# Optimization experiments

Hardware: AMD Instinct MI355X
Metric: run time of the kernel (lower is better)

The kernel has to match this reference:

```python
import jax, jax.numpy as jnp
import numpy as np

B, D, K = 8, 128, 7          # batch, num objects, per-object feature
Q = 256                      # question embedding size
G0, G1 = 511, 512            # g-layer sizes
F1, F2, OUT = 512, 1024, 16  # f-layer sizes


def setup_inputs() -> dict:
    key = jax.random.key(0)
    ks = jax.random.split(key, 14)
    def lin(kw, kb, fan_in, fan_out):
        lim = 1.0 / np.sqrt(fan_in)
        w = jax.random.uniform(kw, (fan_in, fan_out), jnp.float32, -lim, lim)
        b = jax.random.uniform(kb, (fan_out,), jnp.float32, -lim, lim)
        return w, b
    x = jax.random.normal(ks[0], (B, D, K), jnp.float32)
    qst = jax.random.normal(ks[1], (B, Q), jnp.float32)
    g0_w, g0_b = lin(ks[2], ks[3], 2 * K, G0)
    g1_w, g1_b = lin(ks[4], ks[5], G0 + Q, G1)
    f1_w, f1_b = lin(ks[6], ks[7], G1, F1)
    f2_w, f2_b = lin(ks[8], ks[9], F1, F2)
    f3_w, f3_b = lin(ks[10], ks[11], F2, OUT)
    return {"x": x, "qst": qst,
            "g0_w": g0_w, "g0_b": g0_b, "g1_w": g1_w, "g1_b": g1_b,
            "f1_w": f1_w, "f1_b": f1_b, "f2_w": f2_w, "f2_b": f2_b,
            "f3_w": f3_w, "f3_b": f3_b}


def reference(x, qst, g0_w, g0_b, g1_w, g1_b, f1_w, f1_b, f2_w, f2_b, f3_w, f3_b):
    b, d, k = x.shape
    # all-pairs: torch x_i[b,a,c,:]=x[b,c,:], x_j[b,a,c,:]=x[b,a,:]
    x_i = jnp.broadcast_to(x[:, None, :, :], (b, d, d, k))
    x_j = jnp.broadcast_to(x[:, :, None, :], (b, d, d, k))
    pairs = jnp.concatenate([x_i, x_j], axis=-1)            # (b,d,d,2k)
    h = jax.nn.relu(pairs @ g0_w + g0_b)                    # (b,d,d,G0)
    q = jnp.broadcast_to(qst[:, None, None, :], (b, d, d, qst.shape[-1]))
    h = jnp.concatenate([h, q], axis=-1)                    # (b,d,d,G0+Q)
    h = jax.nn.relu(h @ g1_w + g1_b)                        # (b,d,d,G1)
    x_g = h.sum(axis=(1, 2))                                # sum over d^2 pairs -> (b,G1)
    f = jax.nn.relu(x_g @ f1_w + f1_b)
    f = jax.nn.relu(f @ f2_w + f2_b)                        # dropout = identity (eval)
    logits = f @ f3_w + f3_b
    return jax.nn.log_softmax(logits, axis=1)
```

## Files before the change

### kernel.cpp

```cpp
#include <hip/hip_runtime.h>
#include <hip/hip_bf16.h>

#define B_  8
#define D_  128
#define K_  7
#define Q_  256
#define G0_ 511
#define G0P 512
#define G1_ 512
#define F1_ 512
#define F2_ 1024
#define OUT_ 16

typedef __bf16 bf16x8 __attribute__((ext_vector_type(8)));
typedef float  f32x4  __attribute__((ext_vector_type(4)));

#define GL2LDS(g, l) __builtin_amdgcn_global_load_lds(                        \
    (const __attribute__((address_space(1))) void*)(g),                       \
    (__attribute__((address_space(3))) void*)(l), 16, 0, 0)

__global__ void k_prep(const float* __restrict__ x, const float* __restrict__ g0w,
                       const float* __restrict__ g0b, const float* __restrict__ qst,
                       const float* __restrict__ g1w, const float* __restrict__ g1b,
                       const float* __restrict__ f1w, const float* __restrict__ f2w,
                       const float* __restrict__ f3w,
                       float* __restrict__ u, float* __restrict__ v,
                       __bf16* __restrict__ w1t, float* __restrict__ qterm,
                       float* __restrict__ xg, float* __restrict__ f1t,
                       float* __restrict__ f2t, float* __restrict__ f3t) {
    const int blk = blockIdx.x;
    const int t   = threadIdx.x;
    if (blk < 1024) {
        __shared__ float xs[8];
        if (t < K_) xs[t] = x[blk * K_ + t];
        __syncthreads();
        #pragma unroll
        for (int h = 0; h < 2; ++h) {
            const int g = t + h * 256;
            float su = 0.f, sv = 0.f;
            if (g < G0_) {
                #pragma unroll
                for (int k = 0; k < K_; ++k) {
                    su += xs[k] * g0w[k * G0_ + g];
                    sv += xs[k] * g0w[(K_ + k) * G0_ + g];
                }
                su += g0b[g];
            }
            u[blk * G0P + g] = (g < G0_) ? su : 0.f;
            v[blk * G0P + g] = (g < G0_) ? sv : 0.f;
        }
    } else if (blk < 1280) {
        __shared__ __bf16 tile[32][33];
        const int bb = blk - 1024;
        const int bx = bb & 15, by = bb >> 4;
        const int r = t >> 5, c = t & 31;
        #pragma unroll
        for (int i = 0; i < 4; ++i) {
            const int k = by * 32 + r + i * 8;
            const int n = bx * 32 + c;
            tile[r + i * 8][c] = (__bf16)((k < G0_) ? g1w[k * G1_ + n] : 0.f);
        }
        __syncthreads();
        #pragma unroll
        for (int i = 0; i < 4; ++i) {
            const int n = bx * 32 + r + i * 8;
            const int cc = (c >> 3) & 3, j = c & 7;
            const int slot = cc ^ ((n >> 1) & 3);
            w1t[by * 16384 + n * 32 + slot * 8 + j] = tile[c][r + i * 8];
        }
    } else if (blk < 1312) {
        __shared__ float qs[256];
        __shared__ float red[2][128];
        const int qb = blk - 1280;
        const int b = qb >> 2, nb = (qb & 3) << 7;
        qs[t] = qst[b * Q_ + t];
        __syncthreads();
        const int n = nb + (t & 127);
        const int qh = (t >> 7) * 128;
        float s = 0.f;
        #pragma unroll 8
        for (int q = 0; q < 128; ++q)
            s += qs[qh + q] * g1w[(G0_ + qh + q) * G1_ + n];
        red[t >> 7][t & 127] = s;
        __syncthreads();
        if (t < 128)
            qterm[b * G1_ + nb + t] = red[0][t] + red[1][t] + g1b[nb + t];
    } else if (blk < 1320) {
        const int b = blk - 1312;
        xg[b * G1_ + t] = 0.f;
        xg[b * G1_ + 256 + t] = 0.f;
    } else if (blk < 1576) {
        __shared__ float tile[32][33];
        const int j = blk - 1320;
        const int bo = j & 15, bk = j >> 4;
        const int r = t >> 5, c = t & 31;
        #pragma unroll
        for (int i = 0; i < 4; ++i)
            tile[r + i * 8][c] = f1w[(bk * 32 + r + i * 8) * F1_ + bo * 32 + c];
        __syncthreads();
        #pragma unroll
        for (int i = 0; i < 4; ++i)
            f1t[(bo * 32 + r + i * 8) * G1_ + bk * 32 + c] = tile[c][r + i * 8];
    } else if (blk < 2088) {
        __shared__ float tile[32][33];
        const int j = blk - 1576;
        const int bo = j & 31, bk = j >> 5;
        const int r = t >> 5, c = t & 31;
        #pragma unroll
        for (int i = 0; i < 4; ++i)
            tile[r + i * 8][c] = f2w[(bk * 32 + r + i * 8) * F2_ + bo * 32 + c];
        __syncthreads();
        #pragma unroll
        for (int i = 0; i < 4; ++i)
            f2t[(bo * 32 + r + i * 8) * F1_ + bk * 32 + c] = tile[c][r + i * 8];
    } else {
        const int k = (blk - 2088) * 256 + t;
        float4 r0 = *(const float4*)(f3w + k * OUT_);
        float4 r1 = *(const float4*)(f3w + k * OUT_ + 4);
        float4 r2 = *(const float4*)(f3w + k * OUT_ + 8);
        float4 r3 = *(const float4*)(f3w + k * OUT_ + 12);
        const float rr[16] = {r0.x,r0.y,r0.z,r0.w, r1.x,r1.y,r1.z,r1.w,
                              r2.x,r2.y,r2.z,r2.w, r3.x,r3.y,r3.z,r3.w};
        #pragma unroll
        for (int o = 0; o < 16; ++o) f3t[o * F2_ + k] = rr[o];
    }
}

__global__ __launch_bounds__(256, 2)
void k_pair(const float* __restrict__ u, const float* __restrict__ v,
            const __bf16* __restrict__ w1t, const float* __restrict__ qterm,
            float* __restrict__ xg) {
    __shared__ float  v_a[512];
    __shared__ __bf16 At[2][4096];
    __shared__ __bf16 Bt[3][8192];
    __shared__ float  ebuf[4][128];

    const int bid  = blockIdx.x;
    const int b    = bid >> 8;
    const int a    = (bid >> 1) & 127;
    const int nbase = (bid & 1) << 8;
    const int tid  = threadIdx.x;
    const int wave = tid >> 6, lane = tid & 63;
    const int quad = lane >> 4, l15 = lane & 15;
    const int nloc = (wave >> 1) * 128;
    const int mtg  = (wave & 1) * 4;
    const int swz  = (l15 >> 1) & 3;

    const int iw0 = wave * 4;
    const __bf16* gsrc = w1t + (size_t)(nbase + iw0 * 16 + (lane >> 2)) * 32
                             + (lane & 3) * 8;

    const int sm = tid >> 1;
    const int sk = (tid & 1) << 4;
    const float* urow = u + (b * D_ + sm) * G0P + sk;
    const int woff = (sm >> 4) * 512 + (sk >> 3) * 128 + (sm & 15) * 8;

    f32x4 acc[4][8];
    #pragma unroll
    for (int mt = 0; mt < 4; ++mt)
        #pragma unroll
        for (int nt = 0; nt < 8; ++nt)
            acc[mt][nt] = (f32x4){0.f, 0.f, 0.f, 0.f};

    float4 u0, u1, u2, u3;
    auto load_u = [&](int kq) {
        const float* p = urow + kq * 32;
        u0 = *(const float4*)p;       u1 = *(const float4*)(p + 4);
        u2 = *(const float4*)(p + 8); u3 = *(const float4*)(p + 12);
    };
    auto stage_B = [&](int buf, int kq) {
        const __bf16* g = gsrc + kq * 16384;
        __bf16* l = &Bt[buf][iw0 * 512];
        #pragma unroll
        for (int j = 0; j < 4; ++j)
            GL2LDS(g + j * 512, l + j * 512);
    };
    auto write_A = [&](int buf, int kq) {
        const float* vp = v_a + kq * 32 + sk;
        const float4 v0 = *(const float4*)vp,       v1 = *(const float4*)(vp + 4);
        const float4 v2 = *(const float4*)(vp + 8), v3 = *(const float4*)(vp + 12);
        bf16x8 h0, h1;
        h0[0] = (__bf16)fmaxf(u0.x + v0.x, 0.f);
        h0[1] = (__bf16)fmaxf(u0.y + v0.y, 0.f);
        h0[2] = (__bf16)fmaxf(u0.z + v0.z, 0.f);
        h0[3] = (__bf16)fmaxf(u0.w + v0.w, 0.f);
        h0[4] = (__bf16)fmaxf(u1.x + v1.x, 0.f);
        h0[5] = (__bf16)fmaxf(u1.y + v1.y, 0.f);
        h0[6] = (__bf16)fmaxf(u1.z + v1.z, 0.f);
        h0[7] = (__bf16)fmaxf(u1.w + v1.w, 0.f);
        h1[0] = (__bf16)fmaxf(u2.x + v2.x, 0.f);
        h1[1] = (__bf16)fmaxf(u2.y + v2.y, 0.f);
        h1[2] = (__bf16)fmaxf(u2.z + v2.z, 0.f);
        h1[3] = (__bf16)fmaxf(u2.w + v2.w, 0.f);
        h1[4] = (__bf16)fmaxf(u3.x + v3.x, 0.f);
        h1[5] = (__bf16)fmaxf(u3.y + v3.y, 0.f);
        h1[6] = (__bf16)fmaxf(u3.z + v3.z, 0.f);
        h1[7] = (__bf16)fmaxf(u3.w + v3.w, 0.f);
        __bf16* w = &At[buf][woff];
        *(bf16x8*)w = h0;
        *(bf16x8*)(w + 128) = h1;
    };

    float4 vq;
    if (tid < 128) vq = *(const float4*)(v + (b * D_ + a) * G0P + tid * 4);
    load_u(0);
    asm volatile("" ::: "memory");
    stage_B(0, 0);
    stage_B(1, 1);
    if (tid < 128) *(float4*)(v_a + tid * 4) = vq;
    asm volatile("s_waitcnt lgkmcnt(0)\n\ts_barrier" ::: "memory");
    write_A(0, 0);
    asm volatile("s_waitcnt vmcnt(4) lgkmcnt(0)\n\ts_barrier" ::: "memory");

    int bcur = 0, bnxt = 1, bstg = 2;
    for (int kq = 0; kq < 16; ++kq) {
        const int abuf = kq & 1;
        if (kq < 15) load_u(kq + 1);
        asm volatile("" ::: "memory");
        if (kq < 14) stage_B(bstg, kq + 2);
        bf16x8 af[4];
        #pragma unroll
        for (int mt = 0; mt < 4; ++mt)
            af[mt] = *(const bf16x8*)&At[abuf][(mtg + mt) * 512 + lane * 8];
        bf16x8 bfr[8];
        const __bf16* btb = &Bt[bcur][(nloc + l15) * 32 + ((quad ^ swz) << 3)];
        #pragma unroll
        for (int nt = 0; nt < 8; ++nt)
            bfr[nt] = *(const bf16x8*)(btb + nt * 512);
        #pragma unroll
        for (int mt = 0; mt < 4; ++mt)
            #pragma unroll
            for (int nt = 0; nt < 8; ++nt)
                acc[mt][nt] = __builtin_amdgcn_mfma_f32_16x16x32_bf16(
                    af[mt], bfr[nt], acc[mt][nt], 0, 0, 0);
        if (kq < 15) write_A(abuf ^ 1, kq + 1);
        asm volatile("s_waitcnt lgkmcnt(0)\n\ts_barrier" ::: "memory");
        const int t3 = bcur; bcur = bnxt; bnxt = bstg; bstg = t3;
    }

    #pragma unroll
    for (int nt = 0; nt < 8; ++nt) {
        const float q = qterm[b * G1_ + nbase + nloc + nt * 16 + l15];
        float s = 0.f;
        #pragma unroll
        for (int mt = 0; mt < 4; ++mt)
            #pragma unroll
            for (int r = 0; r < 4; ++r)
                s += fmaxf(acc[mt][nt][r] + q, 0.f);
        s += __shfl_xor(s, 16, 64);
        s += __shfl_xor(s, 32, 64);
        if (quad == 0) ebuf[wave][nt * 16 + l15] = s;
    }
    __syncthreads();
    {
        const int grp = tid >> 7, nl = tid & 127;
        const float sv = ebuf[grp * 2][nl] + ebuf[grp * 2 + 1][nl];
        atomicAdd(xg + b * G1_ + nbase + grp * 128 + nl, sv);
    }
}

__global__ void k_f1(const float* __restrict__ xg, const float* __restrict__ f1t,
                     const float* __restrict__ f1b, float* __restrict__ s1g) {
    const int wave = threadIdx.x >> 6, lane = threadIdx.x & 63;
    const int id = blockIdx.x * 4 + wave;
    const int b = id >> 9, oo = id & 511;
    const float* xr = xg + b * G1_ + lane * 8;
    const float* wr = f1t + oo * G1_ + lane * 8;
    const float4 a0 = *(const float4*)xr, a1 = *(const float4*)(xr + 4);
    const float4 b0 = *(const float4*)wr, b1 = *(const float4*)(wr + 4);
    float s = a0.x*b0.x + a0.y*b0.y + a0.z*b0.z + a0.w*b0.w
            + a1.x*b1.x + a1.y*b1.y + a1.z*b1.z + a1.w*b1.w;
    #pragma unroll
    for (int off = 32; off >= 1; off >>= 1) s += __shfl_xor(s, off, 64);
    if (lane == 0) s1g[b * F1_ + oo] = fmaxf(s + f1b[oo], 0.f);
}

__global__ void k_f2(const float* __restrict__ s1g, const float* __restrict__ f2t,
                     const float* __restrict__ f2b, float* __restrict__ s2g) {
    const int wave = threadIdx.x >> 6, lane = threadIdx.x & 63;
    const int id = blockIdx.x * 4 + wave;
    const int b = id >> 10, oo = id & 1023;
    const float* xr = s1g + b * F1_ + lane * 8;
    const float* wr = f2t + oo * F1_ + lane * 8;
    const float4 a0 = *(const float4*)xr, a1 = *(const float4*)(xr + 4);
    const float4 b0 = *(const float4*)wr, b1 = *(const float4*)(wr + 4);
    float s = a0.x*b0.x + a0.y*b0.y + a0.z*b0.z + a0.w*b0.w
            + a1.x*b1.x + a1.y*b1.y + a1.z*b1.z + a1.w*b1.w;
    #pragma unroll
    for (int off = 32; off >= 1; off >>= 1) s += __shfl_xor(s, off, 64);
    if (lane == 0) s2g[b * F2_ + oo] = fmaxf(s + f2b[oo], 0.f);
}

__global__ void k_f3(const float* __restrict__ s2g, const float* __restrict__ f3t,
                     const float* __restrict__ f3b, float* __restrict__ out) {
    const int b = blockIdx.x, t = threadIdx.x;
    const int wave = t >> 6, lane = t & 63;
    __shared__ float lg[16];
    float4 xs[4];
    #pragma unroll
    for (int j = 0; j < 4; ++j)
        xs[j] = *(const float4*)(s2g + b * F2_ + lane * 16 + j * 4);
    #pragma unroll
    for (int oi = 0; oi < 4; ++oi) {
        const int o = wave * 4 + oi;
        const float* wr = f3t + o * F2_ + lane * 16;
        float s = 0.f;
        #pragma unroll
        for (int j = 0; j < 4; ++j) {
            const float4 w = *(const float4*)(wr + j * 4);
            s += xs[j].x*w.x + xs[j].y*w.y + xs[j].z*w.z + xs[j].w*w.w;
        }
        #pragma unroll
        for (int off = 32; off >= 1; off >>= 1) s += __shfl_xor(s, off, 64);
        if (lane == 0) lg[o] = s + f3b[o];
    }
    __syncthreads();
    if (t < 16) {
        float m = -1e30f;
        #pragma unroll
        for (int i = 0; i < 16; ++i) m = fmaxf(m, lg[i]);
        float se = 0.f;
        #pragma unroll
        for (int i = 0; i < 16; ++i) se += __expf(lg[i] - m);
        out[b * OUT_ + t] = lg[t] - m - logf(se);
    }
}

extern "C" void kernel_launch(void* const* d_in, const int* in_sizes, int n_in,
                              void* d_out, int out_size, void* d_ws, size_t ws_size,
                              hipStream_t stream) {
    const float* x   = (const float*)d_in[0];
    const float* qst = (const float*)d_in[1];
    const float* g0w = (const float*)d_in[2];
    const float* g0b = (const float*)d_in[3];
    const float* g1w = (const float*)d_in[4];
    const float* g1b = (const float*)d_in[5];
    const float* f1w = (const float*)d_in[6];
    const float* f1b = (const float*)d_in[7];
    const float* f2w = (const float*)d_in[8];
    const float* f2b = (const float*)d_in[9];
    const float* f3w = (const float*)d_in[10];
    const float* f3b = (const float*)d_in[11];

    char* ws = (char*)d_ws;
    float*  u     = (float*)ws;  ws += (size_t)B_ * D_ * G0P * 4;
    float*  v     = (float*)ws;  ws += (size_t)B_ * D_ * G0P * 4;
    __bf16* w1t   = (__bf16*)ws; ws += (size_t)G1_ * G0P * 2;
    float*  qterm = (float*)ws;  ws += (size_t)B_ * G1_ * 4;
    float*  xg    = (float*)ws;  ws += (size_t)B_ * G1_ * 4;
    float*  s1g   = (float*)ws;  ws += (size_t)B_ * F1_ * 4;
    float*  s2g   = (float*)ws;  ws += (size_t)B_ * F2_ * 4;
    float*  f1t   = (float*)ws;  ws += (size_t)F1_ * G1_ * 4;
    float*  f2t   = (float*)ws;  ws += (size_t)F2_ * F1_ * 4;
    float*  f3t   = (float*)ws;  ws += (size_t)OUT_ * F2_ * 4;

    k_prep<<<2092, 256, 0, stream>>>(x, g0w, g0b, qst, g1w, g1b, f1w, f2w, f3w,
                                     u, v, w1t, qterm, xg, f1t, f2t, f3t);
    k_pair<<<B_ * D_ * 2, 256, 0, stream>>>(u, v, w1t, qterm, xg);
    k_f1  <<<1024, 256, 0, stream>>>(xg, f1t, f1b, s1g);
    k_f2  <<<2048, 256, 0, stream>>>(s1g, f2t, f2b, s2g);
    k_f3  <<<B_, 256, 0, stream>>>(s2g, f3t, f3b, (float*)d_out);
}
```

Baseline: 192.2 us.

## Split g1 MFMA k-step into four phases interleaved with LDS loads and staging

The inner k-loop of the fused g1 GEMM is broken into four phases of eight MFMAs each. The global-to-LDS staging, B-fragment LDS reads and v_a reads are spread between the phases. Each phase is bracketed by s_barrier, sched_barrier and s_setprio, so waves alternate between memory issue and MFMA bursts, aiming to overlap LDS and global traffic with matrix math. This adds several extra workgroup barriers per iteration, which may cost more than the overlap gains.

Result: slower. 220.5 us (+14.8%).

```diff
diff --git a/kernel.cpp b/kernel.cpp
--- a/kernel.cpp
+++ b/kernel.cpp
@@ -168,17 +168,10 @@
         u0 = *(const float4*)p;       u1 = *(const float4*)(p + 4);
         u2 = *(const float4*)(p + 8); u3 = *(const float4*)(p + 12);
     };
-    auto stage_B = [&](int buf, int kq) {
-        const __bf16* g = gsrc + kq * 16384;
-        __bf16* l = &Bt[buf][iw0 * 512];
-        #pragma unroll
-        for (int j = 0; j < 4; ++j)
-            GL2LDS(g + j * 512, l + j * 512);
+    auto stage1 = [&](int buf, int kq, int j) {
+        GL2LDS(gsrc + (size_t)kq * 16384 + j * 512, &Bt[buf][iw0 * 512 + j * 512]);
     };
-    auto write_A = [&](int buf, int kq) {
-        const float* vp = v_a + kq * 32 + sk;
-        const float4 v0 = *(const float4*)vp,       v1 = *(const float4*)(vp + 4);
-        const float4 v2 = *(const float4*)(vp + 8), v3 = *(const float4*)(vp + 12);
+    auto write_A = [&](int buf, float4 v0, float4 v1, float4 v2, float4 v3) {
         bf16x8 h0, h1;
         h0[0] = (__bf16)fmaxf(u0.x + v0.x, 0.f);
         h0[1] = (__bf16)fmaxf(u0.y + v0.y, 0.f);
@@ -201,42 +194,96 @@
         *(bf16x8*)(w + 128) = h1;
     };
 
+#define MM(mt, nt, bf) acc[mt][nt] = __builtin_amdgcn_mfma_f32_16x16x32_bf16( \
+        af##mt, bf, acc[mt][nt], 0, 0, 0)
+#define PH_ENTER() do {                                   \
+        asm volatile("s_barrier" ::: "memory");           \
+        __builtin_amdgcn_sched_barrier(0);                \
+        __builtin_amdgcn_s_setprio(1);                    \
+    } while (0)
+#define PH_EXIT() do {                                    \
+        __builtin_amdgcn_s_setprio(0);                    \
+        asm volatile("s_barrier" ::: "memory");           \
+    } while (0)
+
     float4 vq;
     if (tid < 128) vq = *(const float4*)(v + (b * D_ + a) * G0P + tid * 4);
     load_u(0);
     asm volatile("" ::: "memory");
-    stage_B(0, 0);
-    stage_B(1, 1);
+    #pragma unroll
+    for (int j = 0; j < 4; ++j) stage1(0, 0, j);
+    #pragma unroll
+    for (int j = 0; j < 4; ++j) stage1(1, 1, j);
     if (tid < 128) *(float4*)(v_a + tid * 4) = vq;
     asm volatile("s_waitcnt lgkmcnt(0)\n\ts_barrier" ::: "memory");
-    write_A(0, 0);
+    {
+        const float* vp = v_a + sk;
+        write_A(0, *(const float4*)vp, *(const float4*)(vp + 4),
+                   *(const float4*)(vp + 8), *(const float4*)(vp + 12));
+    }
     asm volatile("s_waitcnt vmcnt(4) lgkmcnt(0)\n\ts_barrier" ::: "memory");
 
     int bcur = 0, bnxt = 1, bstg = 2;
     for (int kq = 0; kq < 16; ++kq) {
         const int abuf = kq & 1;
+        const __bf16* atb = &At[abuf][mtg * 512 + lane * 8];
+        const __bf16* btb = &Bt[bcur][(nloc + l15) * 32 + ((quad ^ swz) << 3)];
+        float4 vv0, vv1, vv2, vv3;
+
         if (kq < 15) load_u(kq + 1);
         asm volatile("" ::: "memory");
-        if (kq < 14) stage_B(bstg, kq + 2);
-        bf16x8 af[4];
-        #pragma unroll
-        for (int mt = 0; mt < 4; ++mt)
-            af[mt] = *(const bf16x8*)&At[abuf][(mtg + mt) * 512 + lane * 8];
-        bf16x8 bfr[8];
-        const __bf16* btb = &Bt[bcur][(nloc + l15) * 32 + ((quad ^ swz) << 3)];
-        #pragma unroll
-        for (int nt = 0; nt < 8; ++nt)
-            bfr[nt] = *(const bf16x8*)(btb + nt * 512);
-        #pragma unroll
-        for (int mt = 0; mt < 4; ++mt)
-            #pragma unroll
-            for (int nt = 0; nt < 8; ++nt)
-                acc[mt][nt] = __builtin_amdgcn_mfma_f32_16x16x32_bf16(
-                    af[mt], bfr[nt], acc[mt][nt], 0, 0, 0);
-        if (kq < 15) write_A(abuf ^ 1, kq + 1);
+        if (kq < 14) stage1(bstg, kq + 2, 0);
+        bf16x8 af0 = *(const bf16x8*)(atb);
+        bf16x8 af1 = *(const bf16x8*)(atb + 512);
+        bf16x8 af2 = *(const bf16x8*)(atb + 1024);
+        bf16x8 af3 = *(const bf16x8*)(atb + 1536);
+        bf16x8 b0 = *(const bf16x8*)(btb);
+        bf16x8 b1 = *(const bf16x8*)(btb + 512);
+        PH_ENTER();
+        MM(0, 0, b0); MM(1, 0, b0); MM(2, 0, b0); MM(3, 0, b0);
+        MM(0, 1, b1); MM(1, 1, b1); MM(2, 1, b1); MM(3, 1, b1);
+        PH_EXIT();
+
+        if (kq < 14) stage1(bstg, kq + 2, 1);
+        bf16x8 b2 = *(const bf16x8*)(btb + 1024);
+        bf16x8 b3 = *(const bf16x8*)(btb + 1536);
+        PH_ENTER();
+        MM(0, 2, b2); MM(1, 2, b2); MM(2, 2, b2); MM(3, 2, b2);
+        MM(0, 3, b3); MM(1, 3, b3); MM(2, 3, b3); MM(3, 3, b3);
+        PH_EXIT();
+
+        if (kq < 14) stage1(bstg, kq + 2, 2);
+        bf16x8 b4 = *(const bf16x8*)(btb + 2048);
+        bf16x8 b5 = *(const bf16x8*)(btb + 2560);
+        if (kq < 15) {
+            const float* vp = v_a + (kq + 1) * 32 + sk;
+            vv0 = *(const float4*)vp;
+            vv1 = *(const float4*)(vp + 4);
+        }
+        PH_ENTER();
+        MM(0, 4, b4); MM(1, 4, b4); MM(2, 4, b4); MM(3, 4, b4);
+        MM(0, 5, b5); MM(1, 5, b5); MM(2, 5, b5); MM(3, 5, b5);
+        PH_EXIT();
+
+        if (kq < 14) stage1(bstg, kq + 2, 3);
+        bf16x8 b6 = *(const bf16x8*)(btb + 3072);
+        bf16x8 b7 = *(const bf16x8*)(btb + 3584);
+        if (kq < 15) {
+            const float* vp = v_a + (kq + 1) * 32 + sk;
+            vv2 = *(const float4*)(vp + 8);
+            vv3 = *(const float4*)(vp + 12);
+        }
+        PH_ENTER();
+        MM(0, 6, b6); MM(1, 6, b6); MM(2, 6, b6); MM(3, 6, b6);
+        MM(0, 7, b7); MM(1, 7, b7); MM(2, 7, b7); MM(3, 7, b7);
+        __builtin_amdgcn_s_setprio(0);
+        if (kq < 15) write_A(abuf ^ 1, vv0, vv1, vv2, vv3);
         asm volatile("s_waitcnt lgkmcnt(0)\n\ts_barrier" ::: "memory");
         const int t3 = bcur; bcur = bnxt; bnxt = bstg; bstg = t3;
     }
+#undef MM
+#undef PH_ENTER
+#undef PH_EXIT
 
     #pragma unroll
     for (int nt = 0; nt < 8; ++nt) {
```

## Build pair-GEMM A fragments directly in registers instead of staging through LDS

Applied to the files above, without the earlier changes.

Each wave now loads its own u rows in MFMA fragment order, adds the v row, applies relu and converts to bf16 straight into register A fragments. This removes the shared At buffer along with its LDS writes and reads. It also drops the lgkmcnt wait from the per-iteration barrier and adds sched_barrier fences to pin the order of loads, weight staging and MFMAs. The cost is that waves sharing the same M rows now load u from global memory twice, and more registers are held for the u and A values.

After: 244.9 us. 1.27x slower.

```diff
diff --git a/kernel.cpp b/kernel.cpp
--- a/kernel.cpp
+++ b/kernel.cpp
@@ -131,7 +131,6 @@
             const __bf16* __restrict__ w1t, const float* __restrict__ qterm,
             float* __restrict__ xg) {
     __shared__ float  v_a[512];
-    __shared__ __bf16 At[2][4096];
     __shared__ __bf16 Bt[3][8192];
     __shared__ float  ebuf[4][128];
 
@@ -150,10 +149,7 @@
     const __bf16* gsrc = w1t + (size_t)(nbase + iw0 * 16 + (lane >> 2)) * 32
                              + (lane & 3) * 8;
 
-    const int sm = tid >> 1;
-    const int sk = (tid & 1) << 4;
-    const float* urow = u + (b * D_ + sm) * G0P + sk;
-    const int woff = (sm >> 4) * 512 + (sk >> 3) * 128 + (sm & 15) * 8;
+    const float* ubase = u + (size_t)(b * D_ + mtg * 16 + l15) * G0P + quad * 8;
 
     f32x4 acc[4][8];
     #pragma unroll
@@ -162,81 +158,98 @@
         for (int nt = 0; nt < 8; ++nt)
             acc[mt][nt] = (f32x4){0.f, 0.f, 0.f, 0.f};
 
-    float4 u0, u1, u2, u3;
+    float4 ua0, ub0, ua1, ub1, ua2, ub2, ua3, ub3;
     auto load_u = [&](int kq) {
-        const float* p = urow + kq * 32;
-        u0 = *(const float4*)p;       u1 = *(const float4*)(p + 4);
-        u2 = *(const float4*)(p + 8); u3 = *(const float4*)(p + 12);
+        const float* p0 = ubase + kq * 32;
+        const float* p1 = p0 + 16 * G0P;
+        const float* p2 = p0 + 32 * G0P;
+        const float* p3 = p0 + 48 * G0P;
+        ua0 = *(const float4*)p0; ub0 = *(const float4*)(p0 + 4);
+        ua1 = *(const float4*)p1; ub1 = *(const float4*)(p1 + 4);
+        ua2 = *(const float4*)p2; ub2 = *(const float4*)(p2 + 4);
+        ua3 = *(const float4*)p3; ub3 = *(const float4*)(p3 + 4);
     };
-    auto stage_B = [&](int buf, int kq) {
-        const __bf16* g = gsrc + kq * 16384;
-        __bf16* l = &Bt[buf][iw0 * 512];
-        #pragma unroll
-        for (int j = 0; j < 4; ++j)
-            GL2LDS(g + j * 512, l + j * 512);
+    auto stage1 = [&](int buf, int kq, int j) {
+        GL2LDS(gsrc + (size_t)kq * 16384 + j * 512, &Bt[buf][iw0 * 512 + j * 512]);
     };
-    auto write_A = [&](int buf, int kq) {
-        const float* vp = v_a + kq * 32 + sk;
-        const float4 v0 = *(const float4*)vp,       v1 = *(const float4*)(vp + 4);
-        const float4 v2 = *(const float4*)(vp + 8), v3 = *(const float4*)(vp + 12);
-        bf16x8 h0, h1;
-        h0[0] = (__bf16)fmaxf(u0.x + v0.x, 0.f);
-        h0[1] = (__bf16)fmaxf(u0.y + v0.y, 0.f);
-        h0[2] = (__bf16)fmaxf(u0.z + v0.z, 0.f);
-        h0[3] = (__bf16)fmaxf(u0.w + v0.w, 0.f);
-        h0[4] = (__bf16)fmaxf(u1.x + v1.x, 0.f);
-        h0[5] = (__bf16)fmaxf(u1.y + v1.y, 0.f);
-        h0[6] = (__bf16)fmaxf(u1.z + v1.z, 0.f);
-        h0[7] = (__bf16)fmaxf(u1.w + v1.w, 0.f);
-        h1[0] = (__bf16)fmaxf(u2.x + v2.x, 0.f);
-        h1[1] = (__bf16)fmaxf(u2.y + v2.y, 0.f);
-        h1[2] = (__bf16)fmaxf(u2.z + v2.z, 0.f);
-        h1[3] = (__bf16)fmaxf(u2.w + v2.w, 0.f);
-        h1[4] = (__bf16)fmaxf(u3.x + v3.x, 0.f);
-        h1[5] = (__bf16)fmaxf(u3.y + v3.y, 0.f);
-        h1[6] = (__bf16)fmaxf(u3.z + v3.z, 0.f);
-        h1[7] = (__bf16)fmaxf(u3.w + v3.w, 0.f);
-        __bf16* w = &At[buf][woff];
-        *(bf16x8*)w = h0;
-        *(bf16x8*)(w + 128) = h1;
+
+    bf16x8 afc0, afc1, afc2, afc3;
+#define MAKE_A_ONE(dst, UA, UB)                                     \
+    do { bf16x8 h;                                                  \
+        h[0] = (__bf16)fmaxf(UA.x + va.x, 0.f);                     \
+        h[1] = (__bf16)fmaxf(UA.y + va.y, 0.f);                     \
+        h[2] = (__bf16)fmaxf(UA.z + va.z, 0.f);                     \
+        h[3] = (__bf16)fmaxf(UA.w + va.w, 0.f);                     \
+        h[4] = (__bf16)fmaxf(UB.x + vb.x, 0.f);                     \
+        h[5] = (__bf16)fmaxf(UB.y + vb.y, 0.f);                     \
+        h[6] = (__bf16)fmaxf(UB.z + vb.z, 0.f);                     \
+        h[7] = (__bf16)fmaxf(UB.w + vb.w, 0.f);                     \
+        dst = h; } while (0)
+    auto make_A = [&](int kq) {
+        const float* vp = v_a + kq * 32 + quad * 8;
+        const float4 va = *(const float4*)vp;
+        const float4 vb = *(const float4*)(vp + 4);
+        MAKE_A_ONE(afc0, ua0, ub0);
+        MAKE_A_ONE(afc1, ua1, ub1);
+        MAKE_A_ONE(afc2, ua2, ub2);
+        MAKE_A_ONE(afc3, ua3, ub3);
     };
+
+#define MM(AF, nt) acc_ptr[nt] = __builtin_amdgcn_mfma_f32_16x16x32_bf16(     \
+        AF, bfr[nt], acc_ptr[nt], 0, 0, 0)
 
     float4 vq;
     if (tid < 128) vq = *(const float4*)(v + (b * D_ + a) * G0P + tid * 4);
     load_u(0);
+    __builtin_amdgcn_sched_barrier(0);
     asm volatile("" ::: "memory");
-    stage_B(0, 0);
-    stage_B(1, 1);
+    #pragma unroll
+    for (int j = 0; j < 4; ++j) stage1(0, 0, j);
+    #pragma unroll
+    for (int j = 0; j < 4; ++j) stage1(1, 1, j);
     if (tid < 128) *(float4*)(v_a + tid * 4) = vq;
     asm volatile("s_waitcnt lgkmcnt(0)\n\ts_barrier" ::: "memory");
-    write_A(0, 0);
+    make_A(0);
     asm volatile("s_waitcnt vmcnt(4) lgkmcnt(0)\n\ts_barrier" ::: "memory");
 
     int bcur = 0, bnxt = 1, bstg = 2;
     for (int kq = 0; kq < 16; ++kq) {
-        const int abuf = kq & 1;
         if (kq < 15) load_u(kq + 1);
+        __builtin_amdgcn_sched_barrier(0);
         asm volatile("" ::: "memory");
-        if (kq < 14) stage_B(bstg, kq + 2);
-        bf16x8 af[4];
-        #pragma unroll
-        for (int mt = 0; mt < 4; ++mt)
-            af[mt] = *(const bf16x8*)&At[abuf][(mtg + mt) * 512 + lane * 8];
+        if (kq < 14) {
+            stage1(bstg, kq + 2, 0); stage1(bstg, kq + 2, 1);
+            stage1(bstg, kq + 2, 2); stage1(bstg, kq + 2, 3);
+        }
+        __builtin_amdgcn_sched_barrier(0);
+
+        const __bf16* btb = &Bt[bcur][(nloc + l15) * 32 + ((quad ^ swz) << 3)];
         bf16x8 bfr[8];
-        const __bf16* btb = &Bt[bcur][(nloc + l15) * 32 + ((quad ^ swz) << 3)];
         #pragma unroll
         for (int nt = 0; nt < 8; ++nt)
             bfr[nt] = *(const bf16x8*)(btb + nt * 512);
-        #pragma unroll
-        for (int mt = 0; mt < 4; ++mt)
-            #pragma unroll
-            for (int nt = 0; nt < 8; ++nt)
-                acc[mt][nt] = __builtin_amdgcn_mfma_f32_16x16x32_bf16(
-                    af[mt], bfr[nt], acc[mt][nt], 0, 0, 0);
-        if (kq < 15) write_A(abuf ^ 1, kq + 1);
-        asm volatile("s_waitcnt lgkmcnt(0)\n\ts_barrier" ::: "memory");
+        {
+            f32x4* acc_ptr = &acc[0][0];
+            MM(afc0,0); MM(afc0,1); MM(afc0,2); MM(afc0,3);
+            MM(afc0,4); MM(afc0,5); MM(afc0,6); MM(afc0,7);
+            acc_ptr = &acc[1][0];
+            MM(afc1,0); MM(afc1,1); MM(afc1,2); MM(afc1,3);
+            MM(afc1,4); MM(afc1,5); MM(afc1,6); MM(afc1,7);
+            acc_ptr = &acc[2][0];
+            MM(afc2,0); MM(afc2,1); MM(afc2,2); MM(afc2,3);
+            MM(afc2,4); MM(afc2,5); MM(afc2,6); MM(afc2,7);
+            acc_ptr = &acc[3][0];
+            MM(afc3,0); MM(afc3,1); MM(afc3,2); MM(afc3,3);
+            MM(afc3,4); MM(afc3,5); MM(afc3,6); MM(afc3,7);
+        }
+        __builtin_amdgcn_sched_barrier(0);
+
+        if (kq < 15) make_A(kq + 1);
+        asm volatile("s_barrier" ::: "memory");
         const int t3 = bcur; bcur = bnxt; bnxt = bstg; bstg = t3;
     }
+#undef MM
+#undef MAKE_A_ONE
 
     #pragma unroll
     for (int nt = 0; nt < 8; ++nt) {
```

## Split k_pair block tile across 8 waves with 512 threads

Applied to the files above, without the earlier changes.

The pair GEMM kernel now runs 512 threads (8 waves) per block instead of 256. Each wave owns a 64x64 output tile instead of 64x128, which halves its accumulator registers and its per-wave B fragment loads. A-tile generation and B staging are spread over twice as many threads, and the final reduction is adjusted to match. The aim is more waves in flight to hide LDS and global latency, at the cost of more barrier participants and less MFMA work per wave between syncs.

Result: faster. 177.3 us (-7.7%).

```diff
diff --git a/kernel.cpp b/kernel.cpp
--- a/kernel.cpp
+++ b/kernel.cpp
@@ -126,14 +126,14 @@
     }
 }
 
-__global__ __launch_bounds__(256, 2)
+__global__ __launch_bounds__(512, 4)
 void k_pair(const float* __restrict__ u, const float* __restrict__ v,
             const __bf16* __restrict__ w1t, const float* __restrict__ qterm,
             float* __restrict__ xg) {
     __shared__ float  v_a[512];
     __shared__ __bf16 At[2][4096];
     __shared__ __bf16 Bt[3][8192];
-    __shared__ float  ebuf[4][128];
+    __shared__ float  ebuf[8][64];
 
     const int bid  = blockIdx.x;
     const int b    = bid >> 8;
@@ -142,63 +142,54 @@
     const int tid  = threadIdx.x;
     const int wave = tid >> 6, lane = tid & 63;
     const int quad = lane >> 4, l15 = lane & 15;
-    const int nloc = (wave >> 1) * 128;
-    const int mtg  = (wave & 1) * 4;
+    const int wm   = wave >> 2;
+    const int wn   = wave & 3;
+    const int nloc = wn * 64;
+    const int mtg  = wm * 4;
     const int swz  = (l15 >> 1) & 3;
 
-    const int iw0 = wave * 4;
+    const int iw0 = wave * 2;
     const __bf16* gsrc = w1t + (size_t)(nbase + iw0 * 16 + (lane >> 2)) * 32
                              + (lane & 3) * 8;
 
-    const int sm = tid >> 1;
-    const int sk = (tid & 1) << 4;
-    const float* urow = u + (b * D_ + sm) * G0P + sk;
-    const int woff = (sm >> 4) * 512 + (sk >> 3) * 128 + (sm & 15) * 8;
-
-    f32x4 acc[4][8];
+    const int sm = tid >> 2;
+    const int q8 = tid & 3;
+    const float* urow = u + (size_t)(b * D_ + sm) * G0P + q8 * 8;
+    const int woff = (sm >> 4) * 512 + q8 * 128 + (sm & 15) * 8;
+
+    f32x4 acc[4][4];
     #pragma unroll
     for (int mt = 0; mt < 4; ++mt)
         #pragma unroll
-        for (int nt = 0; nt < 8; ++nt)
+        for (int nt = 0; nt < 4; ++nt)
             acc[mt][nt] = (f32x4){0.f, 0.f, 0.f, 0.f};
 
-    float4 u0, u1, u2, u3;
+    float4 ua, ub;
     auto load_u = [&](int kq) {
         const float* p = urow + kq * 32;
-        u0 = *(const float4*)p;       u1 = *(const float4*)(p + 4);
-        u2 = *(const float4*)(p + 8); u3 = *(const float4*)(p + 12);
+        ua = *(const float4*)p;
+        ub = *(const float4*)(p + 4);
     };
     auto stage_B = [&](int buf, int kq) {
-        const __bf16* g = gsrc + kq * 16384;
+        const __bf16* g = gsrc + (size_t)kq * 16384;
         __bf16* l = &Bt[buf][iw0 * 512];
-        #pragma unroll
-        for (int j = 0; j < 4; ++j)
-            GL2LDS(g + j * 512, l + j * 512);
+        GL2LDS(g, l);
+        GL2LDS(g + 512, l + 512);
     };
     auto write_A = [&](int buf, int kq) {
-        const float* vp = v_a + kq * 32 + sk;
-        const float4 v0 = *(const float4*)vp,       v1 = *(const float4*)(vp + 4);
-        const float4 v2 = *(const float4*)(vp + 8), v3 = *(const float4*)(vp + 12);
-        bf16x8 h0, h1;
-        h0[0] = (__bf16)fmaxf(u0.x + v0.x, 0.f);
-        h0[1] = (__bf16)fmaxf(u0.y + v0.y, 0.f);
-        h0[2] = (__bf16)fmaxf(u0.z + v0.z, 0.f);
-        h0[3] = (__bf16)fmaxf(u0.w + v0.w, 0.f);
-        h0[4] = (__bf16)fmaxf(u1.x + v1.x, 0.f);
-        h0[5] = (__bf16)fmaxf(u1.y + v1.y, 0.f);
-        h0[6] = (__bf16)fmaxf(u1.z + v1.z, 0.f);
-        h0[7] = (__bf16)fmaxf(u1.w + v1.w, 0.f);
-        h1[0] = (__bf16)fmaxf(u2.x + v2.x, 0.f);
-        h1[1] = (__bf16)fmaxf(u2.y + v2.y, 0.f);
-        h1[2] = (__bf16)fmaxf(u2.z + v2.z, 0.f);
-        h1[3] = (__bf16)fmaxf(u2.w + v2.w, 0.f);
-        h1[4] = (__bf16)fmaxf(u3.x + v3.x, 0.f);
-        h1[5] = (__bf16)fmaxf(u3.y + v3.y, 0.f);
-        h1[6] = (__bf16)fmaxf(u3.z + v3.z, 0.f);
-        h1[7] = (__bf16)fmaxf(u3.w + v3.w, 0.f);
-        __bf16* w = &At[buf][woff];
-        *(bf16x8*)w = h0;
-        *(bf16x8*)(w + 128) = h1;
+        const float* vp = v_a + kq * 32 + q8 * 8;
+        const float4 va = *(const float4*)vp;
+        const float4 vb = *(const float4*)(vp + 4);
+        bf16x8 h;
+        h[0] = (__bf16)fmaxf(ua.x + va.x, 0.f);
+        h[1] = (__bf16)fmaxf(ua.y + va.y, 0.f);
+        h[2] = (__bf16)fmaxf(ua.z + va.z, 0.f);
+        h[3] = (__bf16)fmaxf(ua.w + va.w, 0.f);
+        h[4] = (__bf16)fmaxf(ub.x + vb.x, 0.f);
+        h[5] = (__bf16)fmaxf(ub.y + vb.y, 0.f);
+        h[6] = (__bf16)fmaxf(ub.z + vb.z, 0.f);
+        h[7] = (__bf16)fmaxf(ub.w + vb.w, 0.f);
+        *(bf16x8*)&At[buf][woff] = h;
     };
 
     float4 vq;
@@ -210,7 +201,7 @@
     if (tid < 128) *(float4*)(v_a + tid * 4) = vq;
     asm volatile("s_waitcnt lgkmcnt(0)\n\ts_barrier" ::: "memory");
     write_A(0, 0);
-    asm volatile("s_waitcnt vmcnt(4) lgkmcnt(0)\n\ts_barrier" ::: "memory");
+    asm volatile("s_waitcnt vmcnt(2) lgkmcnt(0)\n\ts_barrier" ::: "memory");
 
     int bcur = 0, bnxt = 1, bstg = 2;
     for (int kq = 0; kq < 16; ++kq) {
@@ -218,28 +209,31 @@
         if (kq < 15) load_u(kq + 1);
         asm volatile("" ::: "memory");
         if (kq < 14) stage_B(bstg, kq + 2);
+
         bf16x8 af[4];
+        const __bf16* atb = &At[abuf][mtg * 512 + lane * 8];
         #pragma unroll
         for (int mt = 0; mt < 4; ++mt)
-            af[mt] = *(const bf16x8*)&At[abuf][(mtg + mt) * 512 + lane * 8];
-        bf16x8 bfr[8];
+            af[mt] = *(const bf16x8*)(atb + mt * 512);
+        bf16x8 bfr[4];
         const __bf16* btb = &Bt[bcur][(nloc + l15) * 32 + ((quad ^ swz) << 3)];
         #pragma unroll
-        for (int nt = 0; nt < 8; ++nt)
+        for (int nt = 0; nt < 4; ++nt)
             bfr[nt] = *(const bf16x8*)(btb + nt * 512);
         #pragma unroll
         for (int mt = 0; mt < 4; ++mt)
             #pragma unroll
-            for (int nt = 0; nt < 8; ++nt)
+            for (int nt = 0; nt < 4; ++nt)
                 acc[mt][nt] = __builtin_amdgcn_mfma_f32_16x16x32_bf16(
                     af[mt], bfr[nt], acc[mt][nt], 0, 0, 0);
+
         if (kq < 15) write_A(abuf ^ 1, kq + 1);
         asm volatile("s_waitcnt lgkmcnt(0)\n\ts_barrier" ::: "memory");
         const int t3 = bcur; bcur = bnxt; bnxt = bstg; bstg = t3;
     }
 
     #pragma unroll
-    for (int nt = 0; nt < 8; ++nt) {
+    for (int nt = 0; nt < 4; ++nt) {
         const float q = qterm[b * G1_ + nbase + nloc + nt * 16 + l15];
         float s = 0.f;
         #pragma unroll
@@ -252,10 +246,9 @@
         if (quad == 0) ebuf[wave][nt * 16 + l15] = s;
     }
     __syncthreads();
-    {
-        const int grp = tid >> 7, nl = tid & 127;
-        const float sv = ebuf[grp * 2][nl] + ebuf[grp * 2 + 1][nl];
-        atomicAdd(xg + b * G1_ + nbase + grp * 128 + nl, sv);
+    if (tid < 256) {
+        const float sv = ebuf[tid >> 6][tid & 63] + ebuf[4 + (tid >> 6)][tid & 63];
+        atomicAdd(xg + b * G1_ + nbase + tid, sv);
     }
 }
 
@@ -356,7 +349,7 @@
 
     k_prep<<<2092, 256, 0, stream>>>(x, g0w, g0b, qst, g1w, g1b, f1w, f2w, f3w,
                                      u, v, w1t, qterm, xg, f1t, f2t, f3t);
-    k_pair<<<B_ * D_ * 2, 256, 0, stream>>>(u, v, w1t, qterm, xg);
+    k_pair<<<B_ * D_ * 2, 512, 0, stream>>>(u, v, w1t, qterm, xg);
     k_f1  <<<1024, 256, 0, stream>>>(xg, f1t, f1b, s1g);
     k_f2  <<<2048, 256, 0, stream>>>(s1g, f2t, f2b, s2g);
     k_f3  <<<B_, 256, 0, stream>>>(s2g, f3t, f3b, (float*)d_out);
```
